# Kernel tuning notes

Measured on AMD Instinct MI355X. Metric: run time of the kernel, lower is better.

Reference implementation:

```python
import jax, jax.numpy as jnp
import numpy as np

INPUT_DIM = 1024
NUM_HEADS = 16


def setup_inputs() -> dict:
    key = jax.random.key(0)
    k1, k2, k3, k4, k5, k6, k7, k8 = jax.random.split(key, 8)
    bs, seq, dm = 2, 2048, INPUT_DIM
    scale = 1.0 / np.sqrt(dm)
    return {
        "input": jax.random.normal(k1, (bs, seq, dm), dtype=jnp.float32),
        "mask": jax.random.randint(k2, (bs, seq), 0, 2, dtype=jnp.int32),
        "Wq": jax.random.normal(k3, (dm, dm), dtype=jnp.float32) * scale,
        "bq": jax.random.normal(k4, (dm,), dtype=jnp.float32) * 0.01,
        "Wk": jax.random.normal(k5, (dm, dm), dtype=jnp.float32) * scale,
        "bk": jax.random.normal(k6, (dm,), dtype=jnp.float32) * 0.01,
        "Wv": jax.random.normal(k7, (dm, dm), dtype=jnp.float32) * scale,
        "bv": jax.random.normal(k8, (dm,), dtype=jnp.float32) * 0.01,
    }


def reference(input, mask, Wq, bq, Wk, bk, Wv, bv):
    bs, seq, dm = input.shape
    h = NUM_HEADS
    d = dm // h
    # projections: x @ W^T + b (torch Linear convention)
    Q = (input @ Wq.T + bq).reshape(bs, seq, h, d).transpose(0, 2, 1, 3)
    K = (input @ Wk.T + bk).reshape(bs, seq, h, d).transpose(0, 2, 1, 3)
    V = (input @ Wv.T + bv).reshape(bs, seq, h, d).transpose(0, 2, 1, 3)
    # raw scores [bs, h, seq, seq]
    scores = jnp.einsum("bhqd,bhkd->bhqk", Q, K)
    m = mask.astype(jnp.float32).reshape(bs, 1, 1, seq)
    # mask_logits is applied BEFORE the 1/sqrt(d) scaling, as in source
    scores = scores * m + (1.0 - m) * (-1e30)
    scores = scores * (1.0 / np.sqrt(d))
    attn = jax.nn.softmax(scores, axis=-1)  # dropout = identity at eval
    out = jnp.einsum("bhqk,bhkd->bhqd", attn, V)
    return out.transpose(0, 2, 1, 3).reshape(bs, seq, dm)
```

## Files before the change

kernel.cpp:

```cpp
#include <hip/hip_runtime.h>
#include <stdint.h>
#include <stddef.h>

#define SEQ 2048
#define DM  1024
#define NH  16
#define BS  2

typedef __attribute__((ext_vector_type(8)))  __bf16 bf16x8;
typedef __attribute__((ext_vector_type(4)))  __bf16 bf16x4;
typedef __attribute__((ext_vector_type(4)))  float  floatx4;
typedef __attribute__((ext_vector_type(16))) float  floatx16;
typedef __attribute__((ext_vector_type(4)))  unsigned int uintx4;
typedef __attribute__((ext_vector_type(4)))  unsigned short ushortx4;

#if __has_builtin(__builtin_amdgcn_exp2f)
#define EXP2(x) __builtin_amdgcn_exp2f(x)
#else
#define EXP2(x) __expf((x) * 0.6931471805599453f)
#endif

#define QSCALE 0.18033688011112042f

#define GLDS(g, s) __builtin_amdgcn_global_load_lds( \
    (const __attribute__((address_space(1))) void*)(g), \
    (__attribute__((address_space(3))) void*)(s), 16, 0, 0)

__device__ inline unsigned short f2bf(float f) {
  union { float f; unsigned int u; } a; a.f = f;
  unsigned int u = a.u;
  return (unsigned short)((u + 0x7fffu + ((u >> 16) & 1u)) >> 16);
}

__device__ inline bf16x8 ldb8(const unsigned short* p) { return *(const bf16x8*)p; }

__global__ __launch_bounds__(256) void prep(
    const float* __restrict__ x, const float* __restrict__ wq,
    const float* __restrict__ wk, const float* __restrict__ wv,
    const int* __restrict__ mask,
    unsigned short* __restrict__ Xb, unsigned short* __restrict__ Wb,
    unsigned short* __restrict__ mb01) {
  const int bid = blockIdx.x, t = threadIdx.x;
  if (bid < 7168) {
    const float* src; unsigned short* dst; int base;
    if (bid < 4096)      { src = x;  dst = Xb;            base = bid; }
    else if (bid < 5120) { src = wq; dst = Wb;            base = bid - 4096; }
    else if (bid < 6144) { src = wk; dst = Wb + 1048576;  base = bid - 5120; }
    else                 { src = wv; dst = Wb + 2097152;  base = bid - 6144; }
    const int i = base * 256 + t;
    floatx4 v = ((const floatx4*)src)[i];
    ushortx4 o;
    o.x = f2bf(v.x); o.y = f2bf(v.y); o.z = f2bf(v.z); o.w = f2bf(v.w);
    ((ushortx4*)dst)[i] = o;
  } else {
    const int i = (bid - 7168) * 256 + t;
    mb01[i] = mask[i] ? 0x3F80 : 0;
  }
}

__global__ __launch_bounds__(256, 3) void gemm_qkv(
    const unsigned short* __restrict__ Xb, const unsigned short* __restrict__ Wb,
    const float* __restrict__ bq, const float* __restrict__ bk, const float* __restrict__ bv,
    const int* __restrict__ mask,
    unsigned short* __restrict__ Qb, unsigned short* __restrict__ Kb,
    unsigned short* __restrict__ Vt)
{
  __shared__ alignas(16) unsigned short LB[16384];
  const int t = threadIdx.x;
  const int w = t >> 6, l = t & 63;
  const int lm = l & 15, lq = l >> 4;
  const int z = blockIdx.z;
  const size_t m0 = (size_t)blockIdx.y * 128;
  const size_t n0 = (size_t)blockIdx.x * 128;
  const unsigned short* W = Wb + (size_t)z * (1024 * 1024);
  const float* bias = (z == 0) ? bq : ((z == 1) ? bk : bv);
  const float sc = (z == 0) ? QSCALE : 1.0f;

  const int c0 = t, c1 = 256 + t;
  const int row0 = c0 >> 2, row1 = c1 >> 2;
  const int kq0 = (c0 & 3) ^ ((row0 >> 1) & 3);
  const int kq1 = (c1 & 3) ^ ((row1 >> 1) & 3);
  const unsigned short* gA0 = Xb + (m0 + row0) * 1024 + kq0 * 8;
  const unsigned short* gA1 = Xb + (m0 + row1) * 1024 + kq1 * 8;
  const unsigned short* gB0 = W + (n0 + row0) * 1024 + kq0 * 8;
  const unsigned short* gB1 = W + (n0 + row1) * 1024 + kq1 * 8;
  const int la0 = (0 * 256 + w * 64) * 8;
  const int la1 = (1 * 256 + w * 64) * 8;

  const int wr = (w >> 1) * 64, wc = (w & 1) * 64;
  const int sw = (lq ^ ((lm >> 1) & 3)) * 8;
  floatx4 acc[4][4] = {};

  GLDS(gA0, LB + la0);
  GLDS(gA1, LB + la1);
  GLDS(gB0, LB + 8192 + la0);
  GLDS(gB1, LB + 8192 + la1);
  __syncthreads();

  for (int it = 0; it < 32; ++it) {
    const int cur = it & 1;
    if (it < 31) {
      const int kn = (it + 1) * 32;
      const int nb = (cur ^ 1) * 4096;
      GLDS(gA0 + kn, LB + nb + la0);
      GLDS(gA1 + kn, LB + nb + la1);
      GLDS(gB0 + kn, LB + 8192 + nb + la0);
      GLDS(gB1 + kn, LB + 8192 + nb + la1);
    }
    const unsigned short* Ab = LB + cur * 4096;
    const unsigned short* Bb = LB + 8192 + cur * 4096;
    bf16x8 af[4], bfr[4];
#pragma unroll
    for (int i = 0; i < 4; i++) af[i] = ldb8(Ab + (wr + i * 16 + lm) * 32 + sw);
#pragma unroll
    for (int j = 0; j < 4; j++) bfr[j] = ldb8(Bb + (wc + j * 16 + lm) * 32 + sw);
#pragma unroll
    for (int i = 0; i < 4; i++)
#pragma unroll
      for (int j = 0; j < 4; j++)
        acc[i][j] = __builtin_amdgcn_mfma_f32_16x16x32_bf16(af[i], bfr[j], acc[i][j], 0, 0, 0);
    __syncthreads();
  }

  if (z < 2) {
    unsigned short* dst = (z == 0) ? Qb : Kb;
#pragma unroll
    for (int j = 0; j < 4; j++) {
      const int ncol = (int)n0 + wc + j * 16 + lm;
      const float bval = bias[ncol];
#pragma unroll
      for (int i = 0; i < 4; i++)
#pragma unroll
        for (int r = 0; r < 4; r++) {
          const int mrow = (int)m0 + wr + i * 16 + lq * 4 + r;
          dst[(size_t)mrow * 1024 + ncol] = f2bf((acc[i][j][r] + bval) * sc);
        }
    }
  } else {
    float mk[4][4];
#pragma unroll
    for (int i = 0; i < 4; i++)
#pragma unroll
      for (int r = 0; r < 4; r++)
        mk[i][r] = (float)mask[(int)m0 + wr + i * 16 + lq * 4 + r];
#pragma unroll
    for (int j = 0; j < 4; j++) {
      const int nl = wc + j * 16 + lm;
      const float bval = bias[(int)n0 + nl];
#pragma unroll
      for (int i = 0; i < 4; i++)
#pragma unroll
        for (int r = 0; r < 4; r++) {
          const int ml = wr + i * 16 + lq * 4 + r;
          LB[nl * 128 + ((((ml >> 3) ^ (nl & 15)) * 8) | (ml & 7))] =
              f2bf((acc[i][j][r] + bval) * mk[i][r]);
        }
    }
    __syncthreads();
    const int nl = t >> 1, hf = t & 1;
    const int ncol = (int)n0 + nl;
    const int hh = ncol >> 6, dc = ncol & 63;
    const int bb = (int)(m0 >> 11);
    const int s0c = ((int)m0 & 2047) + hf * 64;
    unsigned short* dstp = Vt + (size_t)((bb * 16 + hh) * 64 + dc) * SEQ + s0c;
#pragma unroll
    for (int u = 0; u < 8; ++u) {
      const int phys = (hf * 8 + u) ^ (nl & 15);
      *(uintx4*)(dstp + u * 8) = *(const uintx4*)(LB + nl * 128 + phys * 8);
    }
  }
}

__global__ __launch_bounds__(256, 2) void attn(
    const unsigned short* __restrict__ Qb, const unsigned short* __restrict__ Kb,
    const unsigned short* __restrict__ Vt, const unsigned short* __restrict__ mb01,
    float* __restrict__ out)
{
  __shared__ alignas(16) unsigned short Klds[3][4096];
  __shared__ alignas(16) unsigned short Vlds[3][4096];
  __shared__ alignas(16) unsigned short Plds[4][2048];
  __shared__ alignas(16) unsigned short Mb[2048];

  const int t = threadIdx.x, w = t >> 6, l = t & 63;
  const int ln = l & 31, h = l >> 5;
  const int bid = blockIdx.x;
  const int pp = bid & 31;
  const int b = pp >> 4, head = pp & 15;
  const int q0w = (bid >> 5) * 128 + w * 32;
  const int hoff = head * 64;

  const int sr = l >> 3;
  const int gc = (l & 7) ^ sr;
  const unsigned short* gK[2]; const unsigned short* gV[2];
#pragma unroll
  for (int s2 = 0; s2 < 2; ++s2) {
    const int row = w * 16 + s2 * 8 + sr;
    gK[s2] = Kb + (size_t)(b * SEQ + row) * DM + hoff + gc * 8;
    gV[s2] = Vt + (size_t)((b * NH + head) * 64 + row) * SEQ + gc * 8;
  }

#pragma unroll
  for (int s2 = 0; s2 < 2; ++s2) {
    GLDS(gK[s2],                  &Klds[0][(w * 128 + s2 * 64) * 8]);
    GLDS(gV[s2],                  &Vlds[0][(w * 128 + s2 * 64) * 8]);
    GLDS(gK[s2] + (size_t)64 * DM, &Klds[1][(w * 128 + s2 * 64) * 8]);
    GLDS(gV[s2] + 64,              &Vlds[1][(w * 128 + s2 * 64) * 8]);
  }

  ((uintx4*)Mb)[t] = ((const uintx4*)(mb01 + b * SEQ))[t];

  const unsigned short* Qbase = Qb + (size_t)(b * SEQ + q0w + ln) * DM + hoff + h * 8;
  bf16x8 qf[4];
#pragma unroll
  for (int c = 0; c < 4; ++c) qf[c] = ldb8(Qbase + c * 16);

  const int cc = (ln >> 1) & 3, hb = h ^ (ln & 1);
  int xoff[4];
#pragma unroll
  for (int c = 0; c < 4; ++c) xoff[c] = (c ^ cc) * 16 + hb * 8;

  unsigned short* Pw = &Plds[w][ln * 64];
  floatx16 oacc[2] = {};
  floatx16 tacc = {};

  __syncthreads();

  floatx16 scur[2] = {};
#pragma unroll
  for (int c = 0; c < 4; ++c) {
    const unsigned short* Kc = &Klds[0][ln * 64];
    scur[0] = __builtin_amdgcn_mfma_f32_32x32x16_bf16(ldb8(Kc + xoff[c]),        qf[c], scur[0], 0, 0, 0);
    scur[1] = __builtin_amdgcn_mfma_f32_32x32x16_bf16(ldb8(Kc + 2048 + xoff[c]), qf[c], scur[1], 0, 0, 0);
  }

  int cur = 0, nxt = 1, fut = 2;
  for (int kt = 0; kt < 32; ++kt) {
    if (kt < 30) {
      const int k0n = (kt + 2) * 64;
#pragma unroll
      for (int s2 = 0; s2 < 2; ++s2) {
        GLDS(gK[s2] + (size_t)k0n * DM, &Klds[fut][(w * 128 + s2 * 64) * 8]);
        GLDS(gV[s2] + k0n,              &Vlds[fut][(w * 128 + s2 * 64) * 8]);
      }
    }

    floatx16 snext[2] = {};
    {
      const unsigned short* Kc = &Klds[nxt][ln * 64];
#pragma unroll
      for (int c = 0; c < 4; ++c) {
        snext[0] = __builtin_amdgcn_mfma_f32_32x32x16_bf16(ldb8(Kc + xoff[c]),        qf[c], snext[0], 0, 0, 0);
        snext[1] = __builtin_amdgcn_mfma_f32_32x32x16_bf16(ldb8(Kc + 2048 + xoff[c]), qf[c], snext[1], 0, 0, 0);
      }
    }

#pragma unroll
    for (int kb = 0; kb < 2; ++kb)
#pragma unroll
      for (int g = 0; g < 4; ++g) {
        bf16x4 pk;
#pragma unroll
        for (int r = 0; r < 4; ++r) pk[r] = (__bf16)EXP2(scur[kb][g * 4 + r]);
        *(bf16x4*)(Pw + ((4 * kb + g) ^ (ln & 7)) * 8 + h * 4) = pk;
      }

    bf16x8 pf[4];
#pragma unroll
    for (int c = 0; c < 4; ++c) pf[c] = ldb8(Pw + xoff[c]);

    const int k0 = kt * 64;
#pragma unroll
    for (int c = 0; c < 4; ++c) {
      const bf16x8 mfr = ldb8(Mb + k0 + c * 16 + h * 8);
      tacc = __builtin_amdgcn_mfma_f32_32x32x16_bf16(pf[c], mfr, tacc, 0, 0, 0);
    }

    {
      const unsigned short* Vc = &Vlds[cur][ln * 64];
#pragma unroll
      for (int c = 0; c < 4; ++c) {
        oacc[0] = __builtin_amdgcn_mfma_f32_32x32x16_bf16(pf[c], ldb8(Vc + xoff[c]),        oacc[0], 0, 0, 0);
        oacc[1] = __builtin_amdgcn_mfma_f32_32x32x16_bf16(pf[c], ldb8(Vc + 2048 + xoff[c]), oacc[1], 0, 0, 0);
      }
    }

    __syncthreads();
    scur[0] = snext[0]; scur[1] = snext[1];
    const int tmp = cur; cur = nxt; nxt = fut; fut = tmp;
  }

  float* obase = out + (size_t)(b * SEQ + q0w) * DM + hoff;
#pragma unroll
  for (int r = 0; r < 16; ++r) {
    const int rq = (r & 3) + 8 * (r >> 2) + 4 * h;
    const float iv = __builtin_amdgcn_rcpf(tacc[r]);
    obase[(size_t)rq * DM + ln]      = oacc[0][r] * iv;
    obase[(size_t)rq * DM + 32 + ln] = oacc[1][r] * iv;
  }
}

extern "C" void kernel_launch(void* const* d_in, const int* in_sizes, int n_in,
                              void* d_out, int out_size, void* d_ws, size_t ws_size,
                              hipStream_t stream) {
  const float* x   = (const float*)d_in[0];
  const int*   msk = (const int*)d_in[1];
  const float* Wq  = (const float*)d_in[2];
  const float* bq  = (const float*)d_in[3];
  const float* Wk  = (const float*)d_in[4];
  const float* bk  = (const float*)d_in[5];
  const float* Wv  = (const float*)d_in[6];
  const float* bv  = (const float*)d_in[7];
  float* out = (float*)d_out;

  unsigned short* ws = (unsigned short*)d_ws;
  unsigned short* Xb = ws;
  unsigned short* Wb = Xb + (size_t)4096 * 1024;
  unsigned short* Qb = Wb + (size_t)3 * 1024 * 1024;
  unsigned short* Kb = Qb + (size_t)4096 * 1024;
  unsigned short* Vt = Kb + (size_t)4096 * 1024;
  unsigned short* mb01 = Vt + (size_t)4096 * 1024;

  prep<<<7184, 256, 0, stream>>>(x, Wq, Wk, Wv, msk, Xb, Wb, mb01);

  gemm_qkv<<<dim3(8, 32, 3), 256, 0, stream>>>(Xb, Wb, bq, bk, bv, msk, Qb, Kb, Vt);

  attn<<<512, 256, 0, stream>>>(Qb, Kb, Vt, mb01, out);
}
```

Before: 164.5 us.

## Software-pipeline attention loop: defer PV of previous tile, double-buffer P

```diff
diff --git a/kernel.cpp b/kernel.cpp
--- a/kernel.cpp
+++ b/kernel.cpp
@@ -176,9 +176,9 @@
     const unsigned short* __restrict__ Vt, const unsigned short* __restrict__ mb01,
     float* __restrict__ out)
 {
-  __shared__ alignas(16) unsigned short Klds[3][4096];
+  __shared__ alignas(16) unsigned short Klds[2][4096];
   __shared__ alignas(16) unsigned short Vlds[3][4096];
-  __shared__ alignas(16) unsigned short Plds[4][2048];
+  __shared__ alignas(16) unsigned short Plds[2][4][2048];
   __shared__ alignas(16) unsigned short Mb[2048];
 
   const int t = threadIdx.x, w = t >> 6, l = t & 63;
@@ -201,10 +201,9 @@
 
 #pragma unroll
   for (int s2 = 0; s2 < 2; ++s2) {
-    GLDS(gK[s2],                  &Klds[0][(w * 128 + s2 * 64) * 8]);
-    GLDS(gV[s2],                  &Vlds[0][(w * 128 + s2 * 64) * 8]);
+    GLDS(gK[s2],                   &Klds[0][(w * 128 + s2 * 64) * 8]);
     GLDS(gK[s2] + (size_t)64 * DM, &Klds[1][(w * 128 + s2 * 64) * 8]);
-    GLDS(gV[s2] + 64,              &Vlds[1][(w * 128 + s2 * 64) * 8]);
+    GLDS(gV[s2],                   &Vlds[0][(w * 128 + s2 * 64) * 8]);
   }
 
   ((uintx4*)Mb)[t] = ((const uintx4*)(mb01 + b * SEQ))[t];
@@ -219,34 +218,37 @@
 #pragma unroll
   for (int c = 0; c < 4; ++c) xoff[c] = (c ^ cc) * 16 + hb * 8;
 
-  unsigned short* Pw = &Plds[w][ln * 64];
   floatx16 oacc[2] = {};
   floatx16 tacc = {};
 
   __syncthreads();
 
   floatx16 scur[2] = {};
-#pragma unroll
-  for (int c = 0; c < 4; ++c) {
+  {
     const unsigned short* Kc = &Klds[0][ln * 64];
-    scur[0] = __builtin_amdgcn_mfma_f32_32x32x16_bf16(ldb8(Kc + xoff[c]),        qf[c], scur[0], 0, 0, 0);
-    scur[1] = __builtin_amdgcn_mfma_f32_32x32x16_bf16(ldb8(Kc + 2048 + xoff[c]), qf[c], scur[1], 0, 0, 0);
-  }
-
-  int cur = 0, nxt = 1, fut = 2;
+#pragma unroll
+    for (int c = 0; c < 4; ++c) {
+      scur[0] = __builtin_amdgcn_mfma_f32_32x32x16_bf16(ldb8(Kc + xoff[c]),        qf[c], scur[0], 0, 0, 0);
+      scur[1] = __builtin_amdgcn_mfma_f32_32x32x16_bf16(ldb8(Kc + 2048 + xoff[c]), qf[c], scur[1], 0, 0, 0);
+    }
+  }
+  __syncthreads();
+
   for (int kt = 0; kt < 32; ++kt) {
     if (kt < 30) {
-      const int k0n = (kt + 2) * 64;
-#pragma unroll
-      for (int s2 = 0; s2 < 2; ++s2) {
-        GLDS(gK[s2] + (size_t)k0n * DM, &Klds[fut][(w * 128 + s2 * 64) * 8]);
-        GLDS(gV[s2] + k0n,              &Vlds[fut][(w * 128 + s2 * 64) * 8]);
-      }
+#pragma unroll
+      for (int s2 = 0; s2 < 2; ++s2)
+        GLDS(gK[s2] + (size_t)(kt + 2) * 64 * DM, &Klds[kt & 1][(w * 128 + s2 * 64) * 8]);
+    }
+    if (kt < 31) {
+#pragma unroll
+      for (int s2 = 0; s2 < 2; ++s2)
+        GLDS(gV[s2] + (kt + 1) * 64, &Vlds[(kt + 1) % 3][(w * 128 + s2 * 64) * 8]);
     }
 
     floatx16 snext[2] = {};
-    {
-      const unsigned short* Kc = &Klds[nxt][ln * 64];
+    if (kt < 31) {
+      const unsigned short* Kc = &Klds[(kt + 1) & 1][ln * 64];
 #pragma unroll
       for (int c = 0; c < 4; ++c) {
         snext[0] = __builtin_amdgcn_mfma_f32_32x32x16_bf16(ldb8(Kc + xoff[c]),        qf[c], snext[0], 0, 0, 0);
@@ -254,29 +256,31 @@
       }
     }
 
-#pragma unroll
-    for (int kb = 0; kb < 2; ++kb)
-#pragma unroll
-      for (int g = 0; g < 4; ++g) {
-        bf16x4 pk;
-#pragma unroll
-        for (int r = 0; r < 4; ++r) pk[r] = (__bf16)EXP2(scur[kb][g * 4 + r]);
-        *(bf16x4*)(Pw + ((4 * kb + g) ^ (ln & 7)) * 8 + h * 4) = pk;
+    {
+      unsigned short* Pw = &Plds[kt & 1][w][ln * 64];
+#pragma unroll
+      for (int kb = 0; kb < 2; ++kb)
+#pragma unroll
+        for (int g = 0; g < 4; ++g) {
+          bf16x4 pk;
+#pragma unroll
+          for (int r = 0; r < 4; ++r) pk[r] = (__bf16)EXP2(scur[kb][g * 4 + r]);
+          *(bf16x4*)(Pw + ((4 * kb + g) ^ (ln & 7)) * 8 + h * 4) = pk;
+        }
+    }
+
+    if (kt > 0) {
+      const unsigned short* Pw = &Plds[(kt - 1) & 1][w][ln * 64];
+      const unsigned short* Vc = &Vlds[(kt - 1) % 3][ln * 64];
+      bf16x8 pf[4];
+#pragma unroll
+      for (int c = 0; c < 4; ++c) pf[c] = ldb8(Pw + xoff[c]);
+      const int k0 = (kt - 1) * 64;
+#pragma unroll
+      for (int c = 0; c < 4; ++c) {
+        const bf16x8 mfr = ldb8(Mb + k0 + c * 16 + h * 8);
+        tacc = __builtin_amdgcn_mfma_f32_32x32x16_bf16(pf[c], mfr, tacc, 0, 0, 0);
       }
-
-    bf16x8 pf[4];
-#pragma unroll
-    for (int c = 0; c < 4; ++c) pf[c] = ldb8(Pw + xoff[c]);
-
-    const int k0 = kt * 64;
-#pragma unroll
-    for (int c = 0; c < 4; ++c) {
-      const bf16x8 mfr = ldb8(Mb + k0 + c * 16 + h * 8);
-      tacc = __builtin_amdgcn_mfma_f32_32x32x16_bf16(pf[c], mfr, tacc, 0, 0, 0);
-    }
-
-    {
-      const unsigned short* Vc = &Vlds[cur][ln * 64];
 #pragma unroll
       for (int c = 0; c < 4; ++c) {
         oacc[0] = __builtin_amdgcn_mfma_f32_32x32x16_bf16(pf[c], ldb8(Vc + xoff[c]),        oacc[0], 0, 0, 0);
@@ -284,9 +288,27 @@
       }
     }
 
+    scur[0] = snext[0]; scur[1] = snext[1];
     __syncthreads();
-    scur[0] = snext[0]; scur[1] = snext[1];
-    const int tmp = cur; cur = nxt; nxt = fut; fut = tmp;
+  }
+
+  {
+    const unsigned short* Pw = &Plds[1][w][ln * 64];
+    const unsigned short* Vc = &Vlds[1][ln * 64];
+    bf16x8 pf[4];
+#pragma unroll
+    for (int c = 0; c < 4; ++c) pf[c] = ldb8(Pw + xoff[c]);
+    const int k0 = 31 * 64;
+#pragma unroll
+    for (int c = 0; c < 4; ++c) {
+      const bf16x8 mfr = ldb8(Mb + k0 + c * 16 + h * 8);
+      tacc = __builtin_amdgcn_mfma_f32_32x32x16_bf16(pf[c], mfr, tacc, 0, 0, 0);
+    }
+#pragma unroll
+    for (int c = 0; c < 4; ++c) {
+      oacc[0] = __builtin_amdgcn_mfma_f32_32x32x16_bf16(pf[c], ldb8(Vc + xoff[c]),        oacc[0], 0, 0, 0);
+      oacc[1] = __builtin_amdgcn_mfma_f32_32x32x16_bf16(pf[c], ldb8(Vc + 2048 + xoff[c]), oacc[1], 0, 0, 0);
+    }
   }
 
   float* obase = out + (size_t)(b * SEQ + q0w) * DM + hoff;
```

New measurement: 174.5 us. 6.1% more time.

## Repack P via cross-lane shuffles instead of LDS; stage Q/K stores through LDS

Applied to the files above, without the earlier changes.

```diff
diff --git a/kernel.cpp b/kernel.cpp
--- a/kernel.cpp
+++ b/kernel.cpp
@@ -126,15 +126,24 @@
     unsigned short* dst = (z == 0) ? Qb : Kb;
 #pragma unroll
     for (int j = 0; j < 4; j++) {
-      const int ncol = (int)n0 + wc + j * 16 + lm;
-      const float bval = bias[ncol];
+      const int nl = wc + j * 16 + lm;
+      const float bval = bias[(int)n0 + nl];
 #pragma unroll
       for (int i = 0; i < 4; i++)
 #pragma unroll
         for (int r = 0; r < 4; r++) {
-          const int mrow = (int)m0 + wr + i * 16 + lq * 4 + r;
-          dst[(size_t)mrow * 1024 + ncol] = f2bf((acc[i][j][r] + bval) * sc);
+          const int ml = wr + i * 16 + lq * 4 + r;
+          LB[ml * 128 + ((((nl >> 3) ^ (ml & 15)) * 8) | (nl & 7))] =
+              f2bf((acc[i][j][r] + bval) * sc);
         }
+    }
+    __syncthreads();
+    const int row = t >> 1, hf = t & 1;
+    unsigned short* dstp = dst + (m0 + row) * 1024 + n0 + hf * 64;
+#pragma unroll
+    for (int u = 0; u < 8; ++u) {
+      const int phys = (hf * 8 + u) ^ (row & 15);
+      *(uintx4*)(dstp + u * 8) = *(const uintx4*)(LB + row * 128 + phys * 8);
     }
   } else {
     float mk[4][4];
@@ -178,7 +187,6 @@
 {
   __shared__ alignas(16) unsigned short Klds[3][4096];
   __shared__ alignas(16) unsigned short Vlds[3][4096];
-  __shared__ alignas(16) unsigned short Plds[4][2048];
   __shared__ alignas(16) unsigned short Mb[2048];
 
   const int t = threadIdx.x, w = t >> 6, l = t & 63;
@@ -201,8 +209,8 @@
 
 #pragma unroll
   for (int s2 = 0; s2 < 2; ++s2) {
-    GLDS(gK[s2],                  &Klds[0][(w * 128 + s2 * 64) * 8]);
-    GLDS(gV[s2],                  &Vlds[0][(w * 128 + s2 * 64) * 8]);
+    GLDS(gK[s2],                   &Klds[0][(w * 128 + s2 * 64) * 8]);
+    GLDS(gV[s2],                   &Vlds[0][(w * 128 + s2 * 64) * 8]);
     GLDS(gK[s2] + (size_t)64 * DM, &Klds[1][(w * 128 + s2 * 64) * 8]);
     GLDS(gV[s2] + 64,              &Vlds[1][(w * 128 + s2 * 64) * 8]);
   }
@@ -219,18 +227,19 @@
 #pragma unroll
   for (int c = 0; c < 4; ++c) xoff[c] = (c ^ cc) * 16 + hb * 8;
 
-  unsigned short* Pw = &Plds[w][ln * 64];
   floatx16 oacc[2] = {};
   floatx16 tacc = {};
 
   __syncthreads();
 
-  floatx16 scur[2] = {};
-#pragma unroll
-  for (int c = 0; c < 4; ++c) {
+  floatx16 scur0 = {}, scur1 = {};
+  {
     const unsigned short* Kc = &Klds[0][ln * 64];
-    scur[0] = __builtin_amdgcn_mfma_f32_32x32x16_bf16(ldb8(Kc + xoff[c]),        qf[c], scur[0], 0, 0, 0);
-    scur[1] = __builtin_amdgcn_mfma_f32_32x32x16_bf16(ldb8(Kc + 2048 + xoff[c]), qf[c], scur[1], 0, 0, 0);
+#pragma unroll
+    for (int c = 0; c < 4; ++c) {
+      scur0 = __builtin_amdgcn_mfma_f32_32x32x16_bf16(ldb8(Kc + xoff[c]),        qf[c], scur0, 0, 0, 0);
+      scur1 = __builtin_amdgcn_mfma_f32_32x32x16_bf16(ldb8(Kc + 2048 + xoff[c]), qf[c], scur1, 0, 0, 0);
+    }
   }
 
   int cur = 0, nxt = 1, fut = 2;
@@ -244,48 +253,51 @@
       }
     }
 
-    floatx16 snext[2] = {};
+    floatx16 snext0 = {}, snext1 = {};
     {
       const unsigned short* Kc = &Klds[nxt][ln * 64];
 #pragma unroll
       for (int c = 0; c < 4; ++c) {
-        snext[0] = __builtin_amdgcn_mfma_f32_32x32x16_bf16(ldb8(Kc + xoff[c]),        qf[c], snext[0], 0, 0, 0);
-        snext[1] = __builtin_amdgcn_mfma_f32_32x32x16_bf16(ldb8(Kc + 2048 + xoff[c]), qf[c], snext[1], 0, 0, 0);
+        snext0 = __builtin_amdgcn_mfma_f32_32x32x16_bf16(ldb8(Kc + xoff[c]),        qf[c], snext0, 0, 0, 0);
+        snext1 = __builtin_amdgcn_mfma_f32_32x32x16_bf16(ldb8(Kc + 2048 + xoff[c]), qf[c], snext1, 0, 0, 0);
       }
     }
 
-#pragma unroll
-    for (int kb = 0; kb < 2; ++kb)
-#pragma unroll
-      for (int g = 0; g < 4; ++g) {
-        bf16x4 pk;
-#pragma unroll
-        for (int r = 0; r < 4; ++r) pk[r] = (__bf16)EXP2(scur[kb][g * 4 + r]);
-        *(bf16x4*)(Pw + ((4 * kb + g) ^ (ln & 7)) * 8 + h * 4) = pk;
+    unsigned long long pk[2][4];
+#pragma unroll
+    for (int g = 0; g < 4; ++g) {
+      union { bf16x4 v; unsigned long long u; } p0, p1;
+#pragma unroll
+      for (int r = 0; r < 4; ++r) {
+        p0.v[r] = (__bf16)EXP2(scur0[g * 4 + r]);
+        p1.v[r] = (__bf16)EXP2(scur1[g * 4 + r]);
       }
-
-    bf16x8 pf[4];
-#pragma unroll
-    for (int c = 0; c < 4; ++c) pf[c] = ldb8(Pw + xoff[c]);
-
-    const int k0 = kt * 64;
-#pragma unroll
-    for (int c = 0; c < 4; ++c) {
-      const bf16x8 mfr = ldb8(Mb + k0 + c * 16 + h * 8);
-      tacc = __builtin_amdgcn_mfma_f32_32x32x16_bf16(pf[c], mfr, tacc, 0, 0, 0);
+      pk[0][g] = p0.u; pk[1][g] = p1.u;
     }
 
     {
       const unsigned short* Vc = &Vlds[cur][ln * 64];
+      const int k0 = kt * 64;
 #pragma unroll
       for (int c = 0; c < 4; ++c) {
-        oacc[0] = __builtin_amdgcn_mfma_f32_32x32x16_bf16(pf[c], ldb8(Vc + xoff[c]),        oacc[0], 0, 0, 0);
-        oacc[1] = __builtin_amdgcn_mfma_f32_32x32x16_bf16(pf[c], ldb8(Vc + 2048 + xoff[c]), oacc[1], 0, 0, 0);
+        const int kb = c >> 1, ge = (c & 1) * 2, go = ge + 1;
+        const unsigned long long snd = h ? pk[kb][ge] : pk[kb][go];
+        const unsigned long long rcv =
+            (unsigned long long)__shfl_xor((long long)snd, 32, 64);
+        union { unsigned long long u[2]; bf16x8 v; } fu;
+        fu.u[0] = h ? rcv : pk[kb][ge];
+        fu.u[1] = h ? pk[kb][go] : rcv;
+        const bf16x8 pf = fu.v;
+
+        const bf16x8 mfr = ldb8(Mb + k0 + c * 16 + h * 8);
+        tacc = __builtin_amdgcn_mfma_f32_32x32x16_bf16(pf, mfr, tacc, 0, 0, 0);
+        oacc[0] = __builtin_amdgcn_mfma_f32_32x32x16_bf16(pf, ldb8(Vc + xoff[c]),        oacc[0], 0, 0, 0);
+        oacc[1] = __builtin_amdgcn_mfma_f32_32x32x16_bf16(pf, ldb8(Vc + 2048 + xoff[c]), oacc[1], 0, 0, 0);
       }
     }
 
     __syncthreads();
-    scur[0] = snext[0]; scur[1] = snext[1];
+    scur0 = snext0; scur1 = snext1;
     const int tmp = cur; cur = nxt; nxt = fut; fut = tmp;
   }
 
```

After: 168.5 us. 2.4% more time.
